# Kernel optimization log

Measured on AMD Instinct MI355X. Metric: run time of the kernel, lower is better.

The kernel has to match this reference:

```python
import jax, jax.numpy as jnp
import numpy as np

B, S, D, H, KP, DK = 4, 2048, 1024, 16, 8, 3
DD = D // H
NEG = -1.0e9


def dense(x, W, b):
    return x @ W + b


def dw_conv_causal(x, w, b):
    # x: [B,S,D], w: [DK,D] per-channel kernel, b: [D]; left pad DK-1 zeros -> VALID conv
    xp = jnp.pad(x, ((0, 0), (DK - 1, 0), (0, 0)))
    y = b
    for t in range(DK):
        y = y + xp[:, t:t + S, :] * w[t]
    return y


def split_heads(x):
    return x.reshape(B, S, H, DD).transpose(0, 2, 1, 3)  # [B,H,S,DD]


def pool_causal(x):
    # left pad KP-1 zeros along seq, avg_pool window=stride=KP, VALID
    xp = jnp.pad(x, ((0, 0), (0, 0), (KP - 1, 0), (0, 0)))
    n = (S - 1) // KP + 1  # TF VALID output length
    return xp[:, :, :n * KP, :].reshape(B, H, n, KP, DD).mean(axis=3)


def forward(q, k, v, Wq, bq, Wk, bk, Wv, bv, Wup, bup, Wc, bc,
            wcq, bcq, wck, bck, wcv, bcv):
    norm = float(DD) ** -0.25
    qh = dense(q, Wq, bq) * norm
    kh = dense(k, Wk, bk) * norm
    vh = dense(v, Wv, bv)
    q_in = split_heads(dw_conv_causal(qh, wcq, bcq))
    k_in = split_heads(dw_conv_causal(kh, wck, bck))
    v_in = split_heads(dw_conv_causal(vh, wcv, bcv))
    qp = pool_causal(q_in)  # [B,H,n,DD]
    kp = pool_causal(k_in)
    vp = pool_causal(v_in)
    n = qp.shape[2]
    mask = NEG * (1.0 - jnp.tril(jnp.ones((n, n), dtype=qp.dtype)))
    logits = jnp.einsum('bhnd,bhmd->bhnm', qp, kp) + mask
    attn = jax.nn.softmax(logits, axis=-1)
    out = jnp.einsum('bhnm,bhmd->bhnd', attn, vp)  # [B,H,n,DD]
    up = jnp.repeat(out, KP, axis=2)[:, :, :S, :]  # upsample + crop
    up = dense(up, Wup, bup)
    merged = up.transpose(0, 2, 1, 3).reshape(B, S, D)
    return dense(merged, Wc, bc)


def setup_inputs() -> dict:
    key = jax.random.key(0)
    ks = jax.random.split(key, 20)
    w = lambda i, shp: jax.random.normal(ks[i], shp, dtype=jnp.float32) * 0.02
    return {
        'q': jax.random.normal(ks[0], (B, S, D), dtype=jnp.float32),
        'k': jax.random.normal(ks[1], (B, S, D), dtype=jnp.float32),
        'v': jax.random.normal(ks[2], (B, S, D), dtype=jnp.float32),
        'Wq': w(3, (D, D)), 'bq': jnp.zeros((D,), jnp.float32),
        'Wk': w(4, (D, D)), 'bk': jnp.zeros((D,), jnp.float32),
        'Wv': w(5, (D, D)), 'bv': jnp.zeros((D,), jnp.float32),
        'Wup': w(6, (DD, DD)), 'bup': jnp.zeros((DD,), jnp.float32),
        'Wc': w(7, (D, D)), 'bc': jnp.zeros((D,), jnp.float32),
        'wcq': w(8, (DK, D)), 'bcq': jnp.zeros((D,), jnp.float32),
        'wck': w(9, (DK, D)), 'bck': jnp.zeros((D,), jnp.float32),
        'wcv': w(10, (DK, D)), 'bcv': jnp.zeros((D,), jnp.float32),
    }


def reference(q, k, v, Wq, bq, Wk, bk, Wv, bv, Wup, bup, Wc, bc,
              wcq, bcq, wck, bck, wcv, bcv):
    return forward(q, k, v, Wq, bq, Wk, bk, Wv, bv, Wup, bup, Wc, bc,
                   wcq, bcq, wck, bck, wcv, bcv)
```

## Files before the change

### kernel.cpp

```cpp
#include <hip/hip_runtime.h>
#include <cstdint>
#include <cstddef>

#define Bc  4
#define Sc  2048
#define Dc  1024
#define Hc  16
#define DDc 64
#define Nc  256

typedef unsigned short u16;
typedef unsigned int   u32;
typedef __bf16 bf16_t;
typedef bf16_t bf16x8 __attribute__((ext_vector_type(8)));
typedef float  f32x4  __attribute__((ext_vector_type(4)));

__device__ __forceinline__ u16 f2bf(float x) {
    u32 u = __float_as_uint(x);
    return (u16)((u + 0x7FFFu + ((u >> 16) & 1u)) >> 16);
}
__device__ __forceinline__ u32 pack2(float a, float b) {
    return (u32)f2bf(a) | ((u32)f2bf(b) << 16);
}
__device__ __forceinline__ uint2 pack4(float4 x) {
    return make_uint2(pack2(x.x, x.y), pack2(x.z, x.w));
}
__device__ __forceinline__ float bf2f(u16 x) {
    return __uint_as_float((u32)x << 16);
}
__device__ __forceinline__ float4 f4add(float4 a, float4 b) {
    return make_float4(a.x + b.x, a.y + b.y, a.z + b.z, a.w + b.w);
}

__device__ __forceinline__ void gload_lds16(const void* gp, void* lp) {
    __builtin_amdgcn_global_load_lds(
        reinterpret_cast<const __attribute__((address_space(1))) void*>(
            reinterpret_cast<uintptr_t>(gp)),
        reinterpret_cast<__attribute__((address_space(3))) void*>(
            reinterpret_cast<uintptr_t>(lp)),
        16, 0, 0);
}

__global__ __launch_bounds__(256) void cast_wt4_kernel(
    const float* __restrict__ Wq, const float* __restrict__ Wk,
    const float* __restrict__ Wv, const float* __restrict__ Wc,
    u16* __restrict__ Wt4)
{
    __shared__ float T[64][65];
    const int z = blockIdx.z;
    const float* W = (z == 0) ? Wq : (z == 1) ? Wk : (z == 2) ? Wv : Wc;
    u16* Wt = Wt4 + ((size_t)z << 20);
    const int k0 = blockIdx.y * 64, n0 = blockIdx.x * 64;
    const int c = threadIdx.x & 63, r4 = threadIdx.x >> 6;
    #pragma unroll
    for (int i = 0; i < 16; ++i) {
        int r = i * 4 + r4;
        T[r][c] = W[(size_t)(k0 + r) * 1024 + n0 + c];
    }
    __syncthreads();
    #pragma unroll
    for (int i = 0; i < 16; ++i) {
        int r = i * 4 + r4;
        Wt[(size_t)(n0 + r) * 1024 + k0 + c] = f2bf(T[c][r]);
    }
}

__global__ __launch_bounds__(256) void stage_kernel(
    const float* __restrict__ q, const float* __restrict__ k,
    const float* __restrict__ v, u16* __restrict__ R)
{
    int gid = blockIdx.x * 256 + threadIdx.x;
    int c4 = gid & 255, t = (gid >> 8) & 255, b = (gid >> 16) & 3, inp = gid >> 18;
    const float* src = (inp == 0) ? q : (inp == 1) ? k : v;
    const float4* Xb = (const float4*)(src + (size_t)b * Sc * Dc) + c4;
    const float4* Xr = Xb + ((ptrdiff_t)(t << 3) - 1) * 256;

    float4 r[8];
    if (t > 0) {
        #pragma unroll
        for (int i = 0; i < 8; ++i) r[i] = Xr[(ptrdiff_t)i * 256];
    } else {
        r[0] = make_float4(0.f, 0.f, 0.f, 0.f);
        #pragma unroll
        for (int i = 1; i < 8; ++i) r[i] = Xr[(ptrdiff_t)i * 256];
    }

    float4 s8 = f4add(f4add(f4add(r[0], r[1]), f4add(r[2], r[3])),
                      f4add(f4add(r[4], r[5]), f4add(r[6], r[7])));

    size_t s0 = ((size_t)(inp * 3) << 20) + (((u32)(b * 256 + t)) << 10) + c4 * 4;
    *(uint2*)(R + s0 + (1u << 20)) = pack4(r[0]);
    *(uint2*)(R + s0 + (2u << 20)) = pack4(r[1]);
    if (t < 255) *(uint2*)(R + s0 + 1024) = pack4(s8);
    if (t == 0)  *(uint2*)(R + s0) = make_uint2(0u, 0u);
}

__global__ __launch_bounds__(256) void gemm_sec(
    u16* __restrict__ Rall, const u16* __restrict__ Wt4)
{
    __shared__ __align__(16) u16 As[128 * 32];
    __shared__ __align__(16) u16 Bs[128 * 32];

    const int tid  = threadIdx.x;
    const int lane = tid & 63;
    const int wv   = tid >> 6;
    const int z    = blockIdx.z;
    const int inp  = z / 3;
    const int m0   = blockIdx.y * 128;
    const int n0   = blockIdx.x * 128;

    const char* Ab = (const char*)(Rall + ((size_t)z << 20));
    const char* Bb = (const char*)(Wt4 + ((size_t)inp << 20));

    const int wm   = (wv & 1) * 64;
    const int wn   = (wv >> 1) * 64;
    const int mi   = lane & 15;
    const int quad = lane >> 4;

    f32x4 acc[4][4];
    #pragma unroll
    for (int i = 0; i < 4; ++i)
        #pragma unroll
        for (int j = 0; j < 4; ++j)
            acc[i][j] = (f32x4){0.f, 0.f, 0.f, 0.f};

    const int ra0 = tid >> 2, cb = (tid & 3) * 16;
    char* AsB = (char*)As;
    char* BsB = (char*)Bs;

    for (int k0 = 0; k0 < 1024; k0 += 32) {
        const size_t kb = (size_t)k0 * 2;
        gload_lds16(Ab + ((size_t)(m0 + ra0)      << 11) + kb + cb, AsB + wv * 1024);
        gload_lds16(Ab + ((size_t)(m0 + 64 + ra0) << 11) + kb + cb, AsB + 4096 + wv * 1024);
        gload_lds16(Bb + ((size_t)(n0 + ra0)      << 11) + kb + cb, BsB + wv * 1024);
        gload_lds16(Bb + ((size_t)(n0 + 64 + ra0) << 11) + kb + cb, BsB + 4096 + wv * 1024);
        __syncthreads();

        bf16x8 af[4], bfr[4];
        #pragma unroll
        for (int i = 0; i < 4; ++i)
            af[i] = *reinterpret_cast<const bf16x8*>(&As[(wm + i * 16 + mi) * 32 + quad * 8]);
        #pragma unroll
        for (int j = 0; j < 4; ++j)
            bfr[j] = *reinterpret_cast<const bf16x8*>(&Bs[(wn + j * 16 + mi) * 32 + quad * 8]);

        #pragma unroll
        for (int i = 0; i < 4; ++i)
            #pragma unroll
            for (int j = 0; j < 4; ++j)
                acc[i][j] = __builtin_amdgcn_mfma_f32_16x16x32_bf16(af[i], bfr[j], acc[i][j], 0, 0, 0);

        __syncthreads();
    }

    u16* Cs = Rall + ((size_t)z << 20);
    #pragma unroll
    for (int j = 0; j < 4; ++j) {
        const int col = n0 + wn + j * 16 + mi;
        #pragma unroll
        for (int i = 0; i < 4; ++i) {
            const int row = m0 + wm + i * 16 + quad * 4;
            #pragma unroll
            for (int r = 0; r < 4; ++r)
                Cs[(size_t)(row + r) * 1024 + col] = f2bf(acc[i][j][r]);
        }
    }
}

__global__ __launch_bounds__(256) void combine_kernel(
    const u16* __restrict__ Y,
    const float* __restrict__ wcq, const float* __restrict__ wck, const float* __restrict__ wcv,
    const float* __restrict__ bcq, const float* __restrict__ bck, const float* __restrict__ bcv,
    const float* __restrict__ bq,  const float* __restrict__ bk,  const float* __restrict__ bv,
    u16* __restrict__ qb, u16* __restrict__ kb, u16* __restrict__ vt)
{
    int gid = blockIdx.x * 256 + threadIdx.x;
    int c = gid & 1023, t = (gid >> 10) & 255, b = (gid >> 18) & 3, inp = gid >> 20;
    const float* wc = (inp == 0) ? wcq : (inp == 1) ? wck : wcv;
    const float* bconv = (inp == 0) ? bcq : (inp == 1) ? bck : bcv;
    const float* bl = (inp == 0) ? bq : (inp == 1) ? bk : bv;
    const float nrm = (inp == 2) ? 1.0f : 0.35355339059327373f;

    float w0 = wc[c], w1 = wc[1024 + c], w2 = wc[2048 + c];
    float sumw = w0 + w1 + w2, w12 = w1 + w2;

    u32 lo = gid & 0xFFFFFu;
    size_t z0 = (size_t)(inp * 3) << 20;
    float Y0  = bf2f(Y[z0 + lo]);
    float Y1  = bf2f(Y[z0 + (1u << 20) + lo]);
    float Y2  = bf2f(Y[z0 + (2u << 20) + lo]);
    float Y1p = (t > 0) ? bf2f(Y[z0 + (1u << 20) + lo - 1024]) : 0.f;
    float Y2p = (t > 0) ? bf2f(Y[z0 + (2u << 20) + lo - 1024]) : 0.f;

    float data = sumw * Y0 + w12 * (Y1 - Y1p) + w2 * (Y2 - Y2p);

    float cnt = (t == 0) ? 1.f : 8.f;
    float n0  = (t == 0) ? 0.f : ((t == 1) ? 7.f : 8.f);
    float n1  = (t == 0) ? 0.f : 8.f;
    float n2  = (t == 0) ? 1.f : 8.f;
    float val = 0.125f * (cnt * bconv[c] + nrm * (bl[c] * (n0 * w0 + n1 * w1 + n2 * w2) + data));

    int h = c >> 6, d = c & 63;
    int bh = b * 16 + h;
    u16 bfv = f2bf(val);
    if (inp == 0)
        qb[(((size_t)bh * 256 + t) << 6) + d] = bfv;
    else if (inp == 1)
        kb[(((size_t)bh * 256 + t) << 6) + d] = bfv;
    else
        vt[(size_t)bh * 80 * 256 + (size_t)d * 256 + t] = bfv;
}

__global__ __launch_bounds__(256) void vpad_kernel(u16* __restrict__ vt)
{
    const int bh = blockIdx.x;
    const int tid = threadIdx.x;
    const int rr = tid >> 4;
    const int c0 = (tid & 15) * 16;
    u32 fill = (rr == 0) ? 0x3F803F80u : 0u;
    uint4 val = make_uint4(fill, fill, fill, fill);
    uint4* p = (uint4*)(vt + (size_t)bh * 80 * 256 + (size_t)(64 + rr) * 256 + c0);
    p[0] = val;
    p[1] = val;
}

__global__ __launch_bounds__(256) void attn_mfma(
    const u16* __restrict__ qb, const u16* __restrict__ kb,
    const u16* __restrict__ vt, float* __restrict__ ao)
{
    __shared__ __align__(16) u16 Ps[4][64 * 72];
    const int bh   = blockIdx.x;
    const int tid  = threadIdx.x;
    const int wv   = tid >> 6;
    const int lane = tid & 63;
    const int mi   = lane & 15;
    const int quad = lane >> 4;

    const u16* Qb = qb + (((size_t)bh * 256 + wv * 64) << 6);
    const u16* Kb = kb + ((size_t)bh << 14);
    const u16* Vt = vt + (size_t)bh * 80 * 256;
    u16* P = Ps[wv];

    bf16x8 qf[4][2];
    #pragma unroll
    for (int it = 0; it < 4; ++it)
        #pragma unroll
        for (int kc = 0; kc < 2; ++kc)
            qf[it][kc] = *(const bf16x8*)(Qb + ((it * 16 + mi) << 6) + kc * 32 + quad * 8);

    f32x4 o[4][5];
    #pragma unroll
    for (int it = 0; it < 4; ++it)
        #pragma unroll
        for (int jn = 0; jn < 5; ++jn)
            o[it][jn] = (f32x4){0.f, 0.f, 0.f, 0.f};

    for (int kt = 0; kt <= wv; ++kt) {
        bf16x8 kf[4][2];
        #pragma unroll
        for (int jt = 0; jt < 4; ++jt)
            #pragma unroll
            for (int kc = 0; kc < 2; ++kc)
                kf[jt][kc] = *(const bf16x8*)(Kb + ((kt * 64 + jt * 16 + mi) << 6) + kc * 32 + quad * 8);

        f32x4 s[4][4];
        #pragma unroll
        for (int it = 0; it < 4; ++it)
            #pragma unroll
            for (int jt = 0; jt < 4; ++jt)
                s[it][jt] = (f32x4){0.f, 0.f, 0.f, 0.f};
        #pragma unroll
        for (int kc = 0; kc < 2; ++kc)
            #pragma unroll
            for (int it = 0; it < 4; ++it)
                #pragma unroll
                for (int jt = 0; jt < 4; ++jt)
                    s[it][jt] = __builtin_amdgcn_mfma_f32_16x16x32_bf16(qf[it][kc], kf[jt][kc], s[it][jt], 0, 0, 0);

        const bool diag = (kt == wv);
        #pragma unroll
        for (int it = 0; it < 4; ++it)
            #pragma unroll
            for (int jt = 0; jt < 4; ++jt)
                #pragma unroll
                for (int r = 0; r < 4; ++r) {
                    int qrow = it * 16 + quad * 4 + r;
                    int kcol = jt * 16 + mi;
                    float e = __expf(s[it][jt][r]);
                    if (diag && kcol > qrow) e = 0.f;
                    P[qrow * 72 + kcol] = f2bf(e);
                }

        bf16x8 pf[4][2];
        #pragma unroll
        for (int it = 0; it < 4; ++it)
            #pragma unroll
            for (int kc = 0; kc < 2; ++kc)
                pf[it][kc] = *(const bf16x8*)(P + (it * 16 + mi) * 72 + kc * 32 + quad * 8);

        bf16x8 vf[5][2];
        #pragma unroll
        for (int jn = 0; jn < 5; ++jn)
            #pragma unroll
            for (int kc = 0; kc < 2; ++kc)
                vf[jn][kc] = *(const bf16x8*)(Vt + (size_t)(jn * 16 + mi) * 256 + kt * 64 + kc * 32 + quad * 8);

        #pragma unroll
        for (int kc = 0; kc < 2; ++kc)
            #pragma unroll
            for (int it = 0; it < 4; ++it)
                #pragma unroll
                for (int jn = 0; jn < 5; ++jn)
                    o[it][jn] = __builtin_amdgcn_mfma_f32_16x16x32_bf16(pf[it][kc], vf[jn][kc], o[it][jn], 0, 0, 0);
    }

    #pragma unroll
    for (int it = 0; it < 4; ++it) {
        float inv[4];
        #pragma unroll
        for (int r = 0; r < 4; ++r) {
            float lv = __shfl(o[it][4][r], (lane & 48));
            inv[r] = 1.0f / lv;
        }
        #pragma unroll
        for (int jn = 0; jn < 4; ++jn)
            #pragma unroll
            for (int r = 0; r < 4; ++r) {
                int row = wv * 64 + it * 16 + quad * 4 + r;
                ao[(((size_t)bh * 256 + row) << 6) + jn * 16 + mi] = o[it][jn][r] * inv[r];
            }
    }
}

__global__ __launch_bounds__(256) void updense_kernel(
    const float* __restrict__ ao, const float* __restrict__ Wup,
    const float* __restrict__ bup, u16* __restrict__ ms)
{
    __shared__ float Ws[64 * 64];
    __shared__ float rows[4 * 64];
    const int tid = threadIdx.x;

    #pragma unroll
    for (int i = 0; i < 4; ++i)
        ((float4*)Ws)[tid + 256 * i] = ((const float4*)Wup)[tid + 256 * i];
    rows[tid] = ao[(size_t)blockIdx.x * 256 + tid];
    __syncthreads();

    const int r = tid >> 6, dp = tid & 63;
    const int R = blockIdx.x * 4 + r;
    const int b = R >> 12;
    const int h = (R >> 8) & 15;
    const int m = R & 255;

    float acc = bup[dp];
    #pragma unroll
    for (int d = 0; d < 64; ++d)
        acc += rows[r * 64 + d] * Ws[d * 64 + dp];

    ms[((size_t)(b * Nc + m) << 10) + h * 64 + dp] = f2bf(acc);
}

__global__ __launch_bounds__(256) void gemm_final(
    const u16* __restrict__ A, const u16* __restrict__ Bt,
    const float* __restrict__ bias, float* __restrict__ out)
{
    __shared__ __align__(16) u16 As[128 * 32];
    __shared__ __align__(16) u16 Bs[128 * 32];

    const int tid  = threadIdx.x;
    const int lane = tid & 63;
    const int wv   = tid >> 6;
    const int m0   = blockIdx.y * 128;
    const int n0   = blockIdx.x * 128;

    const int wm   = (wv & 1) * 64;
    const int wn   = (wv >> 1) * 64;
    const int mi   = lane & 15;
    const int quad = lane >> 4;

    f32x4 acc[4][4];
    #pragma unroll
    for (int i = 0; i < 4; ++i)
        #pragma unroll
        for (int j = 0; j < 4; ++j)
            acc[i][j] = (f32x4){0.f, 0.f, 0.f, 0.f};

    const char* Ab = (const char*)A;
    const char* Bb = (const char*)Bt;
    const int ra0 = tid >> 2, cb = (tid & 3) * 16;
    char* AsB = (char*)As;
    char* BsB = (char*)Bs;

    for (int k0 = 0; k0 < 1024; k0 += 32) {
        const size_t kb = (size_t)k0 * 2;
        gload_lds16(Ab + ((size_t)(m0 + ra0)      << 11) + kb + cb, AsB + wv * 1024);
        gload_lds16(Ab + ((size_t)(m0 + 64 + ra0) << 11) + kb + cb, AsB + 4096 + wv * 1024);
        gload_lds16(Bb + ((size_t)(n0 + ra0)      << 11) + kb + cb, BsB + wv * 1024);
        gload_lds16(Bb + ((size_t)(n0 + 64 + ra0) << 11) + kb + cb, BsB + 4096 + wv * 1024);
        __syncthreads();

        bf16x8 af[4], bfr[4];
        #pragma unroll
        for (int i = 0; i < 4; ++i)
            af[i] = *reinterpret_cast<const bf16x8*>(&As[(wm + i * 16 + mi) * 32 + quad * 8]);
        #pragma unroll
        for (int j = 0; j < 4; ++j)
            bfr[j] = *reinterpret_cast<const bf16x8*>(&Bs[(wn + j * 16 + mi) * 32 + quad * 8]);

        #pragma unroll
        for (int i = 0; i < 4; ++i)
            #pragma unroll
            for (int j = 0; j < 4; ++j)
                acc[i][j] = __builtin_amdgcn_mfma_f32_16x16x32_bf16(af[i], bfr[j], acc[i][j], 0, 0, 0);

        __syncthreads();
    }

    #pragma unroll
    for (int j = 0; j < 4; ++j) {
        const int col = n0 + wn + j * 16 + mi;
        const float bv = bias[col];
        #pragma unroll
        for (int i = 0; i < 4; ++i) {
            const int row = m0 + wm + i * 16 + quad * 4;
            #pragma unroll
            for (int r = 0; r < 4; ++r) {
                const int rr = row + r;
                const int b = rr >> 8, t = rr & 255;
                float val = acc[i][j][r] + bv;
                float* po = out + (((size_t)b * Sc + (t << 3)) << 10) + col;
                #pragma unroll
                for (int rep = 0; rep < 8; ++rep)
                    po[(size_t)rep << 10] = val;
            }
        }
    }
}

extern "C" void kernel_launch(void* const* d_in, const int* in_sizes, int n_in,
                              void* d_out, int out_size, void* d_ws, size_t ws_size,
                              hipStream_t stream) {
    const float* q   = (const float*)d_in[0];
    const float* k   = (const float*)d_in[1];
    const float* v   = (const float*)d_in[2];
    const float* Wq  = (const float*)d_in[3];
    const float* bq  = (const float*)d_in[4];
    const float* Wk  = (const float*)d_in[5];
    const float* bk  = (const float*)d_in[6];
    const float* Wv  = (const float*)d_in[7];
    const float* bv  = (const float*)d_in[8];
    const float* Wup = (const float*)d_in[9];
    const float* bup = (const float*)d_in[10];
    const float* Wc  = (const float*)d_in[11];
    const float* bc  = (const float*)d_in[12];
    const float* wcq = (const float*)d_in[13];
    const float* bcq = (const float*)d_in[14];
    const float* wck = (const float*)d_in[15];
    const float* bck = (const float*)d_in[16];
    const float* wcv = (const float*)d_in[17];
    const float* bcv = (const float*)d_in[18];

    u16* Rall = (u16*)d_out;

    char* wsb = (char*)d_ws;
    u16*   Wt4 = (u16*)wsb;
    u16*   qb  = (u16*)(wsb + 8388608);
    u16*   kb  = (u16*)(wsb + 10485760);
    u16*   vt  = (u16*)(wsb + 12582912);
    float* ao  = (float*)(wsb + 15204352);
    u16*   ms  = (u16*)(wsb + 19398656);

    cast_wt4_kernel<<<dim3(16, 16, 4), 256, 0, stream>>>(Wq, Wk, Wv, Wc, Wt4);
    stage_kernel<<<3072, 256, 0, stream>>>(q, k, v, Rall);
    gemm_sec<<<dim3(8, 8, 9), 256, 0, stream>>>(Rall, Wt4);
    combine_kernel<<<12288, 256, 0, stream>>>(Rall, wcq, wck, wcv, bcq, bck, bcv,
                                              bq, bk, bv, qb, kb, vt);
    vpad_kernel<<<64, 256, 0, stream>>>(vt);
    attn_mfma<<<64, 256, 0, stream>>>(qb, kb, vt, ao);
    updense_kernel<<<(Bc * Hc * Nc) / 4, 256, 0, stream>>>(ao, Wup, bup, ms);
    gemm_final<<<dim3(8, 8), 256, 0, stream>>>(ms, Wt4 + ((size_t)3 << 20), bc, (float*)d_out);
}
```

Before: 284.1 us.

## Split final GEMM from upsample scatter and shrink GEMM tiles

The final GEMM now writes a compact [1024x1024] fp32 result into workspace, using 64x64 tiles on a 16x16 grid instead of 128x128 tiles on 8x8. A separate float4-vectorized kernel then replicates each row eight times into the output. This replaces the scattered 4-byte repeated stores in the GEMM epilogue with coalesced 16-byte writes, and gives more blocks to fill the CUs. In exchange it adds a kernel launch and an extra 4MB round trip through memory, and it reuses the attention output buffer as scratch.

```diff
diff --git a/kernel.cpp b/kernel.cpp
--- a/kernel.cpp
+++ b/kernel.cpp
@@ -360,29 +360,29 @@
     ms[((size_t)(b * Nc + m) << 10) + h * 64 + dp] = f2bf(acc);
 }
 
-__global__ __launch_bounds__(256) void gemm_final(
+__global__ __launch_bounds__(256) void gemm_out(
     const u16* __restrict__ A, const u16* __restrict__ Bt,
-    const float* __restrict__ bias, float* __restrict__ out)
-{
-    __shared__ __align__(16) u16 As[128 * 32];
-    __shared__ __align__(16) u16 Bs[128 * 32];
+    const float* __restrict__ bias, float* __restrict__ C)
+{
+    __shared__ __align__(16) u16 As[64 * 32];
+    __shared__ __align__(16) u16 Bs[64 * 32];
 
     const int tid  = threadIdx.x;
     const int lane = tid & 63;
     const int wv   = tid >> 6;
-    const int m0   = blockIdx.y * 128;
-    const int n0   = blockIdx.x * 128;
-
-    const int wm   = (wv & 1) * 64;
-    const int wn   = (wv >> 1) * 64;
+    const int m0   = blockIdx.y * 64;
+    const int n0   = blockIdx.x * 64;
+
+    const int wm   = (wv >> 1) * 32;
+    const int wn   = (wv & 1) * 32;
     const int mi   = lane & 15;
     const int quad = lane >> 4;
 
-    f32x4 acc[4][4];
-    #pragma unroll
-    for (int i = 0; i < 4; ++i)
-        #pragma unroll
-        for (int j = 0; j < 4; ++j)
+    f32x4 acc[2][2];
+    #pragma unroll
+    for (int i = 0; i < 2; ++i)
+        #pragma unroll
+        for (int j = 0; j < 2; ++j)
             acc[i][j] = (f32x4){0.f, 0.f, 0.f, 0.f};
 
     const char* Ab = (const char*)A;
@@ -393,47 +393,55 @@
 
     for (int k0 = 0; k0 < 1024; k0 += 32) {
         const size_t kb = (size_t)k0 * 2;
-        gload_lds16(Ab + ((size_t)(m0 + ra0)      << 11) + kb + cb, AsB + wv * 1024);
-        gload_lds16(Ab + ((size_t)(m0 + 64 + ra0) << 11) + kb + cb, AsB + 4096 + wv * 1024);
-        gload_lds16(Bb + ((size_t)(n0 + ra0)      << 11) + kb + cb, BsB + wv * 1024);
-        gload_lds16(Bb + ((size_t)(n0 + 64 + ra0) << 11) + kb + cb, BsB + 4096 + wv * 1024);
+        gload_lds16(Ab + ((size_t)(m0 + ra0) << 11) + kb + cb, AsB + wv * 1024);
+        gload_lds16(Bb + ((size_t)(n0 + ra0) << 11) + kb + cb, BsB + wv * 1024);
         __syncthreads();
 
-        bf16x8 af[4], bfr[4];
-        #pragma unroll
-        for (int i = 0; i < 4; ++i)
+        bf16x8 af[2], bfr[2];
+        #pragma unroll
+        for (int i = 0; i < 2; ++i)
             af[i] = *reinterpret_cast<const bf16x8*>(&As[(wm + i * 16 + mi) * 32 + quad * 8]);
         #pragma unroll
-        for (int j = 0; j < 4; ++j)
+        for (int j = 0; j < 2; ++j)
             bfr[j] = *reinterpret_cast<const bf16x8*>(&Bs[(wn + j * 16 + mi) * 32 + quad * 8]);
 
         #pragma unroll
-        for (int i = 0; i < 4; ++i)
-            #pragma unroll
-            for (int j = 0; j < 4; ++j)
+        for (int i = 0; i < 2; ++i)
+            #pragma unroll
+            for (int j = 0; j < 2; ++j)
                 acc[i][j] = __builtin_amdgcn_mfma_f32_16x16x32_bf16(af[i], bfr[j], acc[i][j], 0, 0, 0);
 
         __syncthreads();
     }
 
     #pragma unroll
-    for (int j = 0; j < 4; ++j) {
+    for (int j = 0; j < 2; ++j) {
         const int col = n0 + wn + j * 16 + mi;
         const float bv = bias[col];
         #pragma unroll
-        for (int i = 0; i < 4; ++i) {
+        for (int i = 0; i < 2; ++i) {
             const int row = m0 + wm + i * 16 + quad * 4;
             #pragma unroll
-            for (int r = 0; r < 4; ++r) {
-                const int rr = row + r;
-                const int b = rr >> 8, t = rr & 255;
-                float val = acc[i][j][r] + bv;
-                float* po = out + (((size_t)b * Sc + (t << 3)) << 10) + col;
-                #pragma unroll
-                for (int rep = 0; rep < 8; ++rep)
-                    po[(size_t)rep << 10] = val;
-            }
+            for (int r = 0; r < 4; ++r)
+                C[(size_t)(row + r) * 1024 + col] = acc[i][j][r] + bv;
         }
+    }
+}
+
+__global__ __launch_bounds__(256) void upsample_kernel(
+    const float* __restrict__ C, float* __restrict__ out)
+{
+    const float4* C4  = (const float4*)C;
+    float4*       out4 = (float4*)out;
+    int idx0 = blockIdx.x * 1024 + threadIdx.x;
+    #pragma unroll
+    for (int rep = 0; rep < 4; ++rep) {
+        int o4   = idx0 + rep * 256;
+        int col4 = o4 & 255;
+        int rowo = o4 >> 8;
+        int b    = rowo >> 11;
+        int tc   = (rowo & 2047) >> 3;
+        out4[o4] = C4[(size_t)((b << 8) + tc) * 256 + col4];
     }
 }
 
@@ -469,6 +477,7 @@
     u16*   vt  = (u16*)(wsb + 12582912);
     float* ao  = (float*)(wsb + 15204352);
     u16*   ms  = (u16*)(wsb + 19398656);
+    float* Cf  = ao;
 
     cast_wt4_kernel<<<dim3(16, 16, 4), 256, 0, stream>>>(Wq, Wk, Wv, Wc, Wt4);
     stage_kernel<<<3072, 256, 0, stream>>>(q, k, v, Rall);
@@ -478,5 +487,6 @@
     vpad_kernel<<<64, 256, 0, stream>>>(vt);
     attn_mfma<<<64, 256, 0, stream>>>(qb, kb, vt, ao);
     updense_kernel<<<(Bc * Hc * Nc) / 4, 256, 0, stream>>>(ao, Wup, bup, ms);
-    gemm_final<<<dim3(8, 8), 256, 0, stream>>>(ms, Wt4 + ((size_t)3 << 20), bc, (float*)d_out);
-}
+    gemm_out<<<dim3(16, 16), 256, 0, stream>>>(ms, Wt4 + ((size_t)3 << 20), bc, Cf);
+    upsample_kernel<<<2048, 256, 0, stream>>>(Cf, (float*)d_out);
+}
```

New measurement: 276.4 us. 1.03x faster.
